# Kernel optimization log

Measured on AMD Instinct MI355X. Metric: run time of the kernel, lower is better.

## Reference

```python
import jax, jax.numpy as jnp
import numpy as np

N_NEG = 60
TEMP = 0.07

def _normalize(x, axis):
    n = jnp.sqrt(jnp.sum(x * x, axis=axis, keepdims=True))
    return x / jnp.maximum(n, 1e-12)

def _grid_sample(img, grid):
    # img [B,C,H,W], grid [B,h,w,2] in [-1,1]; bilinear, padding_mode='border', align_corners=False
    B, C, H, W = img.shape
    ix = jnp.clip((grid[..., 0] + 1.0) * (W * 0.5) - 0.5, 0.0, W - 1.0)
    iy = jnp.clip((grid[..., 1] + 1.0) * (H * 0.5) - 0.5, 0.0, H - 1.0)
    x0 = jnp.floor(ix); y0 = jnp.floor(iy)
    x1 = jnp.minimum(x0 + 1.0, W - 1.0); y1 = jnp.minimum(y0 + 1.0, H - 1.0)
    wx = (ix - x0)[:, None]; wy = (iy - y0)[:, None]  # [B,1,h,w]
    imgf = img.reshape(B, C, H * W)
    hh, ww = grid.shape[1], grid.shape[2]
    def gat(yy, xx):
        idx = (yy * W + xx).astype(jnp.int32).reshape(B, 1, hh * ww)
        return jnp.take_along_axis(imgf, idx, axis=2).reshape(B, C, hh, ww)
    v00 = gat(y0, x0); v01 = gat(y0, x1); v10 = gat(y1, x0); v11 = gat(y1, x1)
    return (v00 * (1 - wx) * (1 - wy) + v01 * wx * (1 - wy)
            + v10 * (1 - wx) * wy + v11 * wx * wy)

def _forward(ref_fms, tgt_fms, target_l, target_r, queue):
    b, c, h, w = ref_fms.shape
    s = target_l.shape[-1] // w  # integer downscale factor (nearest interpolate == strided slice)
    disps_l = target_l[:, :, ::s, ::s] / float(s)   # [b,1,h,w]
    disps_r = target_r[:, :, ::s, ::s] / float(s)
    xb = jnp.broadcast_to(jnp.linspace(0.0, 1.0, w), (b, h, w))
    yb = jnp.broadcast_to(jnp.linspace(0.0, 1.0, h)[:, None], (b, h, w))

    def warp(img, disp):
        g = jnp.stack([xb + disp[:, 0] / w, yb], axis=-1)
        return _grid_sample(img, 2.0 * g - 1.0)

    # occlusion / validity mask (detached in the original)
    index = jnp.broadcast_to(jnp.arange(w, dtype=ref_fms.dtype), (b, 1, h, w))
    l2r2l = warp(warp(index, disps_r), -disps_l)
    masko = jnp.abs(index - l2r2l)[:, 0] < 3.0
    mask = masko & (disps_l[:, 0] > 0.0) & (xb - disps_l[:, 0] / w >= 0.0)
    mask = jax.lax.stop_gradient(mask).astype(ref_fms.dtype)  # [b,h,w]

    query = _normalize(ref_fms, 1)
    # positive: warp right feature to left view via disparity
    gpos = jnp.stack([xb - disps_l[:, 0] / w, yb], axis=-1)
    positive = _normalize(_grid_sample(tgt_fms, 2.0 * gpos - 1.0), 1)
    l_pos = jnp.einsum('bchw,bchw->bhw', query, positive)[..., None]

    # negatives: random integer pixel shifts around positive location
    # (no n_neg-fold repeat of tgt_fms; vmap grid_sample over the n axis instead)
    k1, k2 = jax.random.split(jax.random.key(1234))
    mag = jax.random.randint(k1, (b, h, w, N_NEG), 1, 25).astype(ref_fms.dtype)
    sgn = jnp.sign(jax.random.uniform(k2, (b, h, w, N_NEG)) - 0.5).astype(ref_fms.dtype)
    x_right = (xb - disps_l[:, 0] / w) * w
    fx = jnp.mod(x_right[..., None] + mag * sgn, float(w)) / w
    fy = fx / h  # faithful to original code (y coord reuses the normalized x coord)
    grids = jnp.moveaxis(jnp.stack([fx, fy], axis=-1), 3, 0)  # [n,b,h,w,2]
    neg = jax.vmap(lambda g: _grid_sample(tgt_fms, 2.0 * g - 1.0))(grids)  # [n,b,c,h,w]
    neg = _normalize(jnp.moveaxis(neg, 0, -1), 1)  # [b,c,h,w,n]
    l_neg = jnp.einsum('bchw,bchwn->bhwn', query, neg)

    qn = _normalize(queue, 0)  # forward re-normalizes the queue each call
    l_q = jnp.einsum('bchw,ck->bhwk', query, jax.lax.stop_gradient(qn))

    logits = jnp.concatenate([l_pos, l_neg, l_q], axis=-1) * mask[..., None]
    logits = logits.reshape(b * h * w, -1) / TEMP
    # CrossEntropyLoss with all-zero labels (positive is class 0)
    return jnp.mean(-jax.nn.log_softmax(logits, axis=-1)[:, 0])

def setup_inputs():
    key = jax.random.key(0)
    k1, k2, k3, k4, k5 = jax.random.split(key, 5)
    b, c, h, w = 2, 128, 64, 128
    H, W = 4 * h, 4 * w
    return {
        'ref_fms': jax.random.normal(k1, (b, c, h, w), jnp.float32),
        'tgt_fms': jax.random.normal(k2, (b, c, h, w), jnp.float32),
        'target_l': jax.random.uniform(k3, (b, 1, H, W), jnp.float32) * 64.0,
        'target_r': jax.random.uniform(k4, (b, 1, H, W), jnp.float32) * 64.0,
        'queue': jax.random.normal(k5, (c, 6000), jnp.float32),
    }

def reference(ref_fms, tgt_fms, target_l, target_r, queue):
    return _forward(ref_fms, tgt_fms, target_l, target_r, queue)
```

## Files before the change

### kernel.cpp

```cpp
#include <hip/hip_runtime.h>
#include <stdint.h>
#include <math.h>

#define HFM 64
#define WFM 128
#define CFM 128
#define BN 2
#define HWFM (HFM*WFM)
#define NPIX (BN*HWFM)
#define KQ 6000
#define KQP 6144
#define NNEG 60
#define NE (NPIX*NNEG)
#define EHALF_U 491520u
#define MSHIFT 15.0f
#define LOG2E 1.4426950408889634f

typedef _Float16 f16_8 __attribute__((ext_vector_type(8)));
typedef _Float16 f16_2 __attribute__((ext_vector_type(2)));
typedef float f32_4 __attribute__((ext_vector_type(4)));

__host__ __device__ __forceinline__ void threefry2x32(uint32_t k0, uint32_t k1,
                                                      uint32_t x0, uint32_t x1,
                                                      uint32_t* o0, uint32_t* o1) {
  uint32_t ks2 = k0 ^ k1 ^ 0x1BD11BDAu;
  x0 += k0; x1 += k1;
#define TFR(r) { x0 += x1; x1 = (x1 << (r)) | (x1 >> (32 - (r))); x1 ^= x0; }
  TFR(13) TFR(15) TFR(26) TFR(6)
  x0 += k1;  x1 += ks2 + 1u;
  TFR(17) TFR(29) TFR(16) TFR(24)
  x0 += ks2; x1 += k0 + 2u;
  TFR(13) TFR(15) TFR(26) TFR(6)
  x0 += k0;  x1 += k1 + 3u;
  TFR(17) TFR(29) TFR(16) TFR(24)
  x0 += k1;  x1 += ks2 + 4u;
  TFR(13) TFR(15) TFR(26) TFR(6)
  x0 += ks2; x1 += k0 + 5u;
#undef TFR
  *o0 = x0; *o1 = x1;
}

__device__ __forceinline__ void gs_coord(float t, float halfdim, float maxc,
                                         int* i0, int* i1, float* w) {
  float g = 2.0f * t - 1.0f;
  float x = (g + 1.0f) * halfdim - 0.5f;
  x = fminf(fmaxf(x, 0.0f), maxc);
  float f = floorf(x);
  *i0 = (int)f;
  *w = x - f;
  *i1 = (int)fminf(f + 1.0f, maxc);
}

__global__ __launch_bounds__(256) void k_A(
    const float* __restrict__ ref, const float* __restrict__ tgt,
    const float* __restrict__ queue,
    const float* __restrict__ target_l, const float* __restrict__ target_r,
    _Float16* __restrict__ refTf, _Float16* __restrict__ tgtTf,
    _Float16* __restrict__ queueTf, float2* __restrict__ qeb,
    float* __restrict__ maskArr, float* __restrict__ xr,
    double* __restrict__ dacc, int* __restrict__ dctr) {
  __shared__ float tile[64][35];
  int blk = blockIdx.x;
  int tid = threadIdx.x;
  if (blk < 64) {
    int p = blk * 256 + tid;
    int b = p >> 13;
    int rem = p & (HWFM - 1);
    int i = rem >> 7, j = rem & 127;
    const float stepx = 1.0f / 127.0f, stepy = 1.0f / 63.0f;
    float xb = (j == 127) ? 1.0f : j * stepx;
    float yb = (i == 63) ? 1.0f : i * stepy;
    const float* tl = target_l + (size_t)b * 256 * 512;
    const float* tr = target_r + (size_t)b * 256 * 512;
    float dl = tl[(4 * i) * 512 + 4 * j] * 0.25f;
    int y0i, y1i; float wy;
    gs_coord(yb, 32.0f, 63.0f, &y0i, &y1i, &wy);
    float t = xb - dl * (1.0f / 128.0f);
    int x0i, x1i; float wx;
    gs_coord(t, 64.0f, 127.0f, &x0i, &x1i, &wx);
    auto innerv = [&](int y, int x) -> float {
      float xbx = (x == 127) ? 1.0f : x * stepx;
      float drv = tr[(4 * y) * 512 + 4 * x] * 0.25f;
      float ti = xbx + drv * (1.0f / 128.0f);
      float g = 2.0f * ti - 1.0f;
      float ix2 = fminf(fmaxf((g + 1.0f) * 64.0f - 0.5f, 0.0f), 127.0f);
      float x0f = floorf(ix2);
      float wxp = ix2 - x0f;
      float x1f = fminf(x0f + 1.0f, 127.0f);
      return x0f * (1.0f - wxp) + x1f * wxp;
    };
    float v00 = innerv(y0i, x0i), v01 = innerv(y0i, x1i);
    float v10 = innerv(y1i, x0i), v11 = innerv(y1i, x1i);
    float l2r2l = v00 * (1.0f - wx) * (1.0f - wy) + v01 * wx * (1.0f - wy)
                + v10 * (1.0f - wx) * wy + v11 * wx * wy;
    bool masko = fabsf((float)j - l2r2l) < 3.0f;
    bool mk = masko && (dl > 0.0f) && (t >= 0.0f);
    maskArr[p] = mk ? 1.0f : 0.0f;
    xr[p] = t * 128.0f;
  } else if (blk < 88) {
    if (blk == 64 && tid == 0) { *dacc = 0.0; *dctr = 0; }
    int k = (blk - 64) * 256 + tid;
    if (k < KQP) {
      if (k >= KQ) { qeb[k] = make_float2(0.0f, -1000.0f); }
      else {
        float ss = 0.0f;
        for (int c = 0; c < CFM; c++) { float v = queue[c * KQ + k]; ss += v * v; }
        float qi = 1.0f / fmaxf(sqrtf(ss), 1e-12f);
        qeb[k] = make_float2(qi * (LOG2E / 0.07f), -MSHIFT * LOG2E);
      }
    }
  } else if (blk < 472) {
    int q = blk - 88;
    int cy = q / 192, nx = q - cy * 192;
    int n0 = nx * 32, c0 = cy * 64;
    int c = tid >> 2, qq = tid & 3;
    const float* sp = queue + (size_t)(c0 + c) * KQ + n0 + qq * 4;
    if (n0 + 32 <= KQ) {
      float4 v0 = *(const float4*)sp;
      float4 v1 = *(const float4*)(sp + 16);
      tile[c][qq * 4 + 0] = v0.x; tile[c][qq * 4 + 1] = v0.y;
      tile[c][qq * 4 + 2] = v0.z; tile[c][qq * 4 + 3] = v0.w;
      tile[c][qq * 4 + 16] = v1.x; tile[c][qq * 4 + 17] = v1.y;
      tile[c][qq * 4 + 18] = v1.z; tile[c][qq * 4 + 19] = v1.w;
    } else {
#pragma unroll
      for (int k = 0; k < 4; k++) {
        int n = n0 + qq * 4 + k;
        tile[c][qq * 4 + k] = (n < KQ) ? sp[k] : 0.0f;
        tile[c][qq * 4 + 16 + k] = (n + 16 < KQ) ? sp[16 + k] : 0.0f;
      }
    }
    __syncthreads();
    int x = tid >> 3, j8 = tid & 7;
    f16_8 o;
#pragma unroll
    for (int k = 0; k < 8; k++) o[k] = (_Float16)tile[j8 * 8 + k][x];
    *(f16_8*)(queueTf + (size_t)(n0 + x) * CFM + c0 + j8 * 8) = o;
  } else {
    int fblk = blk - 472;
    int z = fblk >> 9, rem2 = fblk & 511;
    int cy = rem2 >> 8, xt = rem2 & 255;
    int x0 = xt * 32, c0 = cy * 64;
    int arr = z >> 1, b = z & 1;
    const float* src = (arr == 0 ? ref : tgt) + (size_t)b * CFM * HWFM;
    _Float16* dst = (arr == 0 ? refTf : tgtTf) + (size_t)b * HWFM * CFM;
    int c = tid >> 2, qq = tid & 3;
    const float* sp = src + (size_t)(c0 + c) * HWFM + x0 + qq * 4;
    float4 v0 = *(const float4*)sp;
    float4 v1 = *(const float4*)(sp + 16);
    tile[c][qq * 4 + 0] = v0.x; tile[c][qq * 4 + 1] = v0.y;
    tile[c][qq * 4 + 2] = v0.z; tile[c][qq * 4 + 3] = v0.w;
    tile[c][qq * 4 + 16] = v1.x; tile[c][qq * 4 + 17] = v1.y;
    tile[c][qq * 4 + 18] = v1.z; tile[c][qq * 4 + 19] = v1.w;
    __syncthreads();
    int x = tid >> 3, j8 = tid & 7;
    f16_8 o;
#pragma unroll
    for (int k = 0; k < 8; k++) o[k] = (_Float16)tile[j8 * 8 + k][x];
    *(f16_8*)(dst + (size_t)(x0 + x) * CFM + c0 + j8 * 8) = o;
  }
}

__global__ __launch_bounds__(256) void k_B(
    const _Float16* __restrict__ refTf, const _Float16* __restrict__ tgtTf,
    _Float16* __restrict__ QTf, float* __restrict__ stats,
    const float* __restrict__ maskArr, const float* __restrict__ xr,
    float* __restrict__ S, float* __restrict__ logit0,
    int* __restrict__ count, int* __restrict__ list) {
  __shared__ int wsum[4];
  int blk = blockIdx.x;
  int tid = threadIdx.x;
  int lane = tid & 63;
  if (blk == 0) {
    int wave = tid >> 6;
    int base_p = tid * 64;
    unsigned long long bits = 0ull;
    const float4* m4 = (const float4*)(maskArr + base_p);
#pragma unroll
    for (int k = 0; k < 16; k++) {
      float4 v = m4[k];
      if (v.x > 0.0f) bits |= 1ull << (4 * k + 0);
      if (v.y > 0.0f) bits |= 1ull << (4 * k + 1);
      if (v.z > 0.0f) bits |= 1ull << (4 * k + 2);
      if (v.w > 0.0f) bits |= 1ull << (4 * k + 3);
    }
    int m = __popcll(bits);
    int scan = m;
#pragma unroll
    for (int off = 1; off < 64; off <<= 1) {
      int n = __shfl_up(scan, off, 64);
      if (lane >= off) scan += n;
    }
    if (lane == 63) wsum[wave] = scan;
    __syncthreads();
    int wbase = 0;
    for (int w = 0; w < wave; w++) wbase += wsum[w];
    int idx = wbase + scan - m;
    for (int k = 0; k < 64; k++) {
      if ((bits >> k) & 1ull) list[idx++] = base_p + k;
    }
    if (tid == 255) *count = idx;
  } else if (blk < 65) {
    int sub = tid >> 6;
    int xg = (blk - 1) * 4 + sub;
    int b = xg >> 7, x = xg & 127;
    int xp = min(x + 1, 127);
    int c2 = lane * 2;
    int base = b * HWFM;
    f16_2 c0  = *(const f16_2*)(tgtTf + (size_t)(base + x) * CFM + c2);
    f16_2 c1  = *(const f16_2*)(tgtTf + (size_t)(base + WFM + x) * CFM + c2);
    f16_2 c0p = *(const f16_2*)(tgtTf + (size_t)(base + xp) * CFM + c2);
    f16_2 c1p = *(const f16_2*)(tgtTf + (size_t)(base + WFM + xp) * CFM + c2);
    float a0 = (float)c0[0], a1 = (float)c0[1];
    float b0 = (float)c1[0], b1 = (float)c1[1];
    float p0 = (float)c0p[0], p1 = (float)c0p[1];
    float q0 = (float)c1p[0], q1 = (float)c1p[1];
    float s[7];
    s[0] = a0 * a0 + a1 * a1;
    s[1] = a0 * b0 + a1 * b1;
    s[2] = b0 * b0 + b1 * b1;
    s[3] = a0 * p0 + a1 * p1;
    s[4] = a0 * q0 + a1 * q1;
    s[5] = b0 * p0 + b1 * p1;
    s[6] = b0 * q0 + b1 * q1;
#pragma unroll
    for (int o = 32; o; o >>= 1)
#pragma unroll
      for (int k = 0; k < 7; k++) s[k] += __shfl_xor(s[k], o, 64);
    if (lane == 0) {
      float* st = stats + (size_t)xg * 8;
#pragma unroll
      for (int k = 0; k < 7; k++) st[k] = s[k];
      st[7] = 0.0f;
    }
  } else {
    int wave = tid >> 6;
    int p = (blk - 65) * 4 + wave;
    float mk = maskArr[p];
    if (mk == 0.0f) return;
    int b = p >> 13;
    int rem = p & (HWFM - 1);
    int i = rem >> 7;
    const float stepy = 1.0f / 63.0f;
    float yb = (i == 63) ? 1.0f : i * stepy;
    float t = xr[p] * (1.0f / 128.0f);
    int y0i, y1i; float wy;
    gs_coord(yb, 32.0f, 63.0f, &y0i, &y1i, &wy);
    int x0i, x1i; float wx;
    gs_coord(t, 64.0f, 127.0f, &x0i, &x1i, &wx);

    int c2 = lane * 2;
    f16_2 q2 = *(const f16_2*)(refTf + (size_t)p * CFM + c2);
    int bo = b * HWFM;
    f16_2 a2 = *(const f16_2*)(tgtTf + (size_t)(bo + y0i * WFM + x0i) * CFM + c2);
    f16_2 b2 = *(const f16_2*)(tgtTf + (size_t)(bo + y0i * WFM + x1i) * CFM + c2);
    f16_2 cc2 = *(const f16_2*)(tgtTf + (size_t)(bo + y1i * WFM + x0i) * CFM + c2);
    f16_2 d2 = *(const f16_2*)(tgtTf + (size_t)(bo + y1i * WFM + x1i) * CFM + c2);

    float w00 = (1.0f - wx) * (1.0f - wy), w01 = wx * (1.0f - wy);
    float w10 = (1.0f - wx) * wy,          w11 = wx * wy;
    float q0 = (float)q2[0], q1 = (float)q2[1];
    float v0 = w00 * (float)a2[0] + w01 * (float)b2[0] + w10 * (float)cc2[0] + w11 * (float)d2[0];
    float v1 = w00 * (float)a2[1] + w01 * (float)b2[1] + w10 * (float)cc2[1] + w11 * (float)d2[1];

    float s0 = q0 * q0 + q1 * q1;
    float s1 = q0 * v0 + q1 * v1;
    float s2 = v0 * v0 + v1 * v1;
#pragma unroll
    for (int o = 32; o; o >>= 1) {
      s0 += __shfl_xor(s0, o, 64);
      s1 += __shfl_xor(s1, o, 64);
      s2 += __shfl_xor(s2, o, 64);
    }
    float inv = 1.0f / fmaxf(sqrtf(s0), 1e-12f);
    f16_2 qw; qw[0] = (_Float16)(q0 * inv); qw[1] = (_Float16)(q1 * inv);
    *(f16_2*)(QTf + (size_t)p * CFM + c2) = qw;
    if (lane == 0) {
      float lpos = (s1 * inv) / fmaxf(sqrtf(s2), 1e-12f);
      float lg0 = lpos / 0.07f;
      logit0[p] = lg0;
      S[p] = expf(lg0 - MSHIFT);
    }
  }
}

__global__ __launch_bounds__(256, 4) void k_gemm(
    const _Float16* __restrict__ QTf,
    const _Float16* __restrict__ queueTf,
    const _Float16* __restrict__ tgtTf,
    const float2* __restrict__ qeb,
    float* __restrict__ S, float* __restrict__ D,
    const int* __restrict__ count, const int* __restrict__ list) {
  __shared__ _Float16 Bs[2][64 * CFM];
  __shared__ float Srow[64];
  int tid = threadIdx.x;
  int cnt = *count;
  int split = blockIdx.x & 7;
  int slot0 = (blockIdx.x >> 3) * 64;
  if (slot0 >= cnt) return;
  int wave = tid >> 6, lane = tid & 63;
  int quad = lane >> 4, l16 = lane & 15;
  int wm = wave >> 1, wn = wave & 1;
  int dbatch = split >> 2;
  int dxoff = (split & 3) * 64;

  if (tid < 64) Srow[tid] = 0.0f;

  int lrow = lane >> 4, lchunk = lane & 15;
  auto stage = [&](const _Float16* bsrc, int buf) {
#pragma unroll
    for (int i = 0; i < 4; i++) {
      int rb = wave * 16 + i * 4;
      int r = rb + lrow;
      const _Float16* g = bsrc + (size_t)r * CFM + ((lchunk ^ (r & 7)) << 3);
      __builtin_amdgcn_global_load_lds(
          (const __attribute__((address_space(1))) void*)g,
          (__attribute__((address_space(3))) void*)(&Bs[buf][rb * CFM]),
          16, 0, 0);
    }
  };
  auto bpanel = [&](int ic) -> const _Float16* {
    if (ic < 12) return queueTf + (size_t)(split * 768 + ic * 64) * CFM;
    return tgtTf + ((size_t)dbatch * HWFM + dxoff) * CFM;
  };

  stage(bpanel(0), 0);

  f16_8 Af[2][4];
  int r0 = slot0 + wm * 32;
#pragma unroll
  for (int mt = 0; mt < 2; mt++) {
    int prow = list[min(r0 + mt * 16 + l16, cnt - 1)];
    const _Float16* arow = QTf + (size_t)prow * CFM + quad * 8;
#pragma unroll
    for (int ks = 0; ks < 4; ks++)
      Af[mt][ks] = *(const f16_8*)(arow + ks * 32);
  }
  int pbv[2][4];
#pragma unroll
  for (int mt = 0; mt < 2; mt++)
#pragma unroll
    for (int r = 0; r < 4; r++)
      pbv[mt][r] = list[min(r0 + mt * 16 + quad * 4 + r, cnt - 1)] >> 13;

  __syncthreads();
  int cur = 0;
  float rowsum[2][4] = {{0.0f,0.0f,0.0f,0.0f},{0.0f,0.0f,0.0f,0.0f}};

  for (int ic = 0; ic < 13; ic++) {
    if (ic + 1 < 13) stage(bpanel(ic + 1), cur ^ 1);
    float2 qb[2];
    if (ic < 12) {
      int n0 = split * 768 + ic * 64 + wn * 32;
#pragma unroll
      for (int nt = 0; nt < 2; nt++) qb[nt] = qeb[n0 + nt * 16 + l16];
    }
    f32_4 acc[2][2];
#pragma unroll
    for (int mt = 0; mt < 2; mt++)
#pragma unroll
      for (int nt = 0; nt < 2; nt++)
        acc[mt][nt] = (f32_4){0.0f, 0.0f, 0.0f, 0.0f};
#pragma unroll
    for (int ks = 0; ks < 4; ks++) {
      f16_8 Bk[2];
#pragma unroll
      for (int nt = 0; nt < 2; nt++) {
        int brow = wn * 32 + nt * 16 + l16;
        Bk[nt] = *(const f16_8*)(&Bs[cur][brow * CFM + ((ks * 32 + quad * 8) ^ ((brow & 7) * 8))]);
      }
#pragma unroll
      for (int mt = 0; mt < 2; mt++)
#pragma unroll
        for (int nt = 0; nt < 2; nt++)
          acc[mt][nt] = __builtin_amdgcn_mfma_f32_16x16x32_f16(Af[mt][ks], Bk[nt], acc[mt][nt], 0, 0, 0);
    }
    if (ic < 12) {
#pragma unroll
      for (int nt = 0; nt < 2; nt++)
#pragma unroll
        for (int mt = 0; mt < 2; mt++)
#pragma unroll
          for (int r = 0; r < 4; r++)
            rowsum[mt][r] += exp2f(fmaf(acc[mt][nt][r], qb[nt].x, qb[nt].y));
    } else {
#pragma unroll
      for (int mt = 0; mt < 2; mt++)
#pragma unroll
        for (int nt = 0; nt < 2; nt++)
#pragma unroll
          for (int r = 0; r < 4; r++) {
            int sl = slot0 + wm * 32 + mt * 16 + quad * 4 + r;
            int colL = dxoff + wn * 32 + nt * 16 + l16;
            if (sl < cnt && pbv[mt][r] == dbatch)
              D[(size_t)sl * 256 + colL] = acc[mt][nt][r];
          }
    }
    __syncthreads();
    cur ^= 1;
  }

#pragma unroll
  for (int mt = 0; mt < 2; mt++)
#pragma unroll
    for (int r = 0; r < 4; r++) {
      float vv = rowsum[mt][r];
      vv += __shfl_xor(vv, 1);
      vv += __shfl_xor(vv, 2);
      vv += __shfl_xor(vv, 4);
      vv += __shfl_xor(vv, 8);
      rowsum[mt][r] = vv;
    }
  if (l16 == 0) {
#pragma unroll
    for (int mt = 0; mt < 2; mt++)
#pragma unroll
      for (int r = 0; r < 4; r++)
        atomicAdd(&Srow[wm * 32 + mt * 16 + quad * 4 + r], rowsum[mt][r]);
  }
  __syncthreads();
  if (tid < 64) {
    int pr = slot0 + tid;
    if (pr < cnt) atomicAdd(&S[list[pr]], Srow[tid]);
  }
}

__global__ __launch_bounds__(256) void k_negatives_lite(
    const float* __restrict__ D, const float* __restrict__ stats,
    const float* __restrict__ xr, float* __restrict__ S,
    const int* __restrict__ count, const int* __restrict__ list,
    uint32_t k1a, uint32_t k1b, uint32_t k2a, uint32_t k2b) {
  int tid = threadIdx.x;
  int wave = tid >> 6, lane = tid & 63;
  int cnt = *count;
  int slot = blockIdx.x * 4 + wave;
  if (slot >= cnt) return;
  int p = list[slot];
  int b = p >> 13;
  float esum = 0.0f;
  if (lane < NNEG) {
    uint32_t e = (uint32_t)(p * NNEG + lane);
    uint32_t h0, h1;
    threefry2x32(k1a, k1b, e, e + (uint32_t)NE, &h0, &h1);
    uint32_t off = ((h0 % 24u) * 16u + (h1 % 24u)) % 24u;
    float mag = (float)(1u + off);
    uint32_t ub;
    {
      uint32_t a, bm;
      if (e < EHALF_U) { threefry2x32(k2a, k2b, e, e + EHALF_U, &a, &bm); ub = a; }
      else             { threefry2x32(k2a, k2b, e - EHALF_U, e, &a, &bm); ub = bm; }
    }
    float u = __uint_as_float((ub >> 9) | 0x3F800000u) - 1.0f;
    float sg = (u > 0.5f) ? 1.0f : ((u < 0.5f) ? -1.0f : 0.0f);

    float v = xr[p] + mag * sg;
    float r = fmodf(v, 128.0f);
    if (r < 0.0f) r += 128.0f;
    float fx = r * (1.0f / 128.0f);
    float fy = fx * (1.0f / 64.0f);
    int x0i, x1i, y0i, y1i; float wx, wy;
    gs_coord(fx, 64.0f, 127.0f, &x0i, &x1i, &wx);
    gs_coord(fy, 32.0f, 63.0f, &y0i, &y1i, &wy);

    const float* Dp = D + (size_t)slot * 256;
    float d00 = Dp[x0i], d01 = Dp[x1i];
    float d10 = Dp[128 + x0i], d11 = Dp[128 + x1i];
    float u0 = 1.0f - wy, u1 = wy;
    float dv0 = u0 * d00 + u1 * d10;
    float dv1 = u0 * d01 + u1 * d11;
    float dot = (1.0f - wx) * dv0 + wx * dv1;

    const float* st0 = stats + (size_t)(b * 128 + x0i) * 8;
    const float* st1 = stats + (size_t)(b * 128 + x1i) * 8;
    float4 sa = *(const float4*)st0;
    float4 sb = *(const float4*)(st0 + 4);
    float4 sc = *(const float4*)st1;
    float a0 = u0 * u0, a1 = u0 * u1, a2 = u1 * u1;
    float nB0 = a0 * sa.x + 2.0f * a1 * sa.y + a2 * sa.z;
    float nB1 = a0 * sc.x + 2.0f * a1 * sc.y + a2 * sc.z;
    float cB  = a0 * sa.w + a1 * (sb.x + sb.y) + a2 * sb.z;
    float wx0 = 1.0f - wx;
    float nsq = wx0 * wx0 * nB0 + 2.0f * wx * wx0 * cB + wx * wx * nB1;
    float ln = dot / fmaxf(sqrtf(fmaxf(nsq, 0.0f)), 1e-12f);
    esum = __expf(ln * (1.0f / 0.07f) - MSHIFT);
  }
#pragma unroll
  for (int o = 32; o; o >>= 1) esum += __shfl_xor(esum, o, 64);
  if (lane == 0) atomicAdd(&S[p], esum);
}

__global__ __launch_bounds__(1024) void k_finalize(
    const float* __restrict__ S, const float* __restrict__ logit0,
    const float* __restrict__ maskArr, float* __restrict__ out,
    double* __restrict__ dacc, int* __restrict__ dctr) {
  int tid = threadIdx.x;
  const float cmask = logf(6061.0f);
  int p = blockIdx.x * 1024 + tid;
  float term = (maskArr[p] > 0.0f) ? (logf(S[p]) + MSHIFT - logit0[p]) : cmask;
  double acc = (double)term;
#pragma unroll
  for (int off = 32; off; off >>= 1) acc += __shfl_down(acc, off, 64);
  __shared__ double sd[16];
  if ((tid & 63) == 0) sd[tid >> 6] = acc;
  __syncthreads();
  if (tid == 0) {
    double tot = 0.0;
    for (int w = 0; w < 16; w++) tot += sd[w];
    atomicAdd(dacc, tot);
    __threadfence();
    int old = atomicAdd(dctr, 1);
    if (old == 15) {
      __threadfence();
      out[0] = (float)(*(volatile double*)dacc / (double)NPIX);
    }
  }
}

extern "C" void kernel_launch(void* const* d_in, const int* in_sizes, int n_in,
                              void* d_out, int out_size, void* d_ws, size_t ws_size,
                              hipStream_t stream) {
  const float* ref   = (const float*)d_in[0];
  const float* tgt   = (const float*)d_in[1];
  const float* tl    = (const float*)d_in[2];
  const float* tr    = (const float*)d_in[3];
  const float* queue = (const float*)d_in[4];
  float* out = (float*)d_out;
  float* ws = (float*)d_ws;

  float2* qeb = (float2*)ws;
  float* S    = ws + 12288;
  float* lg0  = ws + 28672;
  float* mk   = ws + 45056;
  float* xr   = ws + 61440;
  int* count  = (int*)(ws + 77824);
  double* dacc = (double*)(ws + 77826);
  int* dctr   = (int*)(ws + 77828);
  int* list   = (int*)(ws + 77840);
  _Float16* QTf     = (_Float16*)(ws + 94464);
  _Float16* queueTf = (_Float16*)(ws + 1143040);
  _Float16* tgtTf   = (_Float16*)(ws + 1536256);
  _Float16* refTf   = (_Float16*)(ws + 2584832);
  float* stats = ws + 3633408;
  float* D     = ws + 3635456;

  uint32_t b0o0, b0o1, b1o0, b1o1;
  threefry2x32(0u, 1234u, 0u, 2u, &b0o0, &b0o1);
  threefry2x32(0u, 1234u, 1u, 3u, &b1o0, &b1o1);
  uint32_t k1a = b0o0, k1b = b1o0, k2a = b0o1, k2b = b1o1;

  k_A<<<dim3(2520), dim3(256), 0, stream>>>(ref, tgt, queue, tl, tr,
                                            refTf, tgtTf, queueTf, qeb, mk, xr,
                                            dacc, dctr);
  k_B<<<dim3(65 + 4096), dim3(256), 0, stream>>>(refTf, tgtTf, QTf, stats,
                                                 mk, xr, S, lg0, count, list);
  k_gemm<<<dim3(2048), dim3(256), 0, stream>>>(QTf, queueTf, tgtTf, qeb,
                                               S, D, count, list);
  k_negatives_lite<<<dim3(NPIX / 4), dim3(256), 0, stream>>>(D, stats, xr, S, count, list,
                                                             k1a, k1b, k2a, k2b);
  k_finalize<<<dim3(16), dim3(1024), 0, stream>>>(S, lg0, mk, out, dacc, dctr);
}
```

Baseline: 115.9 us.

## Parallelize mask compaction with atomics and split GEMM queue columns across more blocks

Replaces the single-block serial compaction of masked pixels with 64 blocks that each use a wave ballot, a popcount prefix and one atomicAdd per wave to append to the active list. The counter is zeroed in k_A. The GEMM grid is doubled to 16 splits per 64-row slot, each covering 384 queue columns instead of 768. Only the first 8 splits also compute the D tile against the target features. The aim is to remove the one-block serial bottleneck in k_B and raise GEMM parallelism, at the cost of a nondeterministic list order and more A-panel reloads.

```diff
diff --git a/kernel.cpp b/kernel.cpp
--- a/kernel.cpp
+++ b/kernel.cpp
@@ -58,7 +58,7 @@
     _Float16* __restrict__ refTf, _Float16* __restrict__ tgtTf,
     _Float16* __restrict__ queueTf, float2* __restrict__ qeb,
     float* __restrict__ maskArr, float* __restrict__ xr,
-    double* __restrict__ dacc, int* __restrict__ dctr) {
+    double* __restrict__ dacc, int* __restrict__ dctr, int* __restrict__ count) {
   __shared__ float tile[64][35];
   int blk = blockIdx.x;
   int tid = threadIdx.x;
@@ -98,7 +98,7 @@
     maskArr[p] = mk ? 1.0f : 0.0f;
     xr[p] = t * 128.0f;
   } else if (blk < 88) {
-    if (blk == 64 && tid == 0) { *dacc = 0.0; *dctr = 0; }
+    if (blk == 64 && tid == 0) { *dacc = 0.0; *dctr = 0; *count = 0; }
     int k = (blk - 64) * 256 + tid;
     if (k < KQP) {
       if (k >= KQ) { qeb[k] = make_float2(0.0f, -1000.0f); }
@@ -167,42 +167,22 @@
     const float* __restrict__ maskArr, const float* __restrict__ xr,
     float* __restrict__ S, float* __restrict__ logit0,
     int* __restrict__ count, int* __restrict__ list) {
-  __shared__ int wsum[4];
   int blk = blockIdx.x;
   int tid = threadIdx.x;
   int lane = tid & 63;
-  if (blk == 0) {
-    int wave = tid >> 6;
-    int base_p = tid * 64;
-    unsigned long long bits = 0ull;
-    const float4* m4 = (const float4*)(maskArr + base_p);
-#pragma unroll
-    for (int k = 0; k < 16; k++) {
-      float4 v = m4[k];
-      if (v.x > 0.0f) bits |= 1ull << (4 * k + 0);
-      if (v.y > 0.0f) bits |= 1ull << (4 * k + 1);
-      if (v.z > 0.0f) bits |= 1ull << (4 * k + 2);
-      if (v.w > 0.0f) bits |= 1ull << (4 * k + 3);
-    }
-    int m = __popcll(bits);
-    int scan = m;
-#pragma unroll
-    for (int off = 1; off < 64; off <<= 1) {
-      int n = __shfl_up(scan, off, 64);
-      if (lane >= off) scan += n;
-    }
-    if (lane == 63) wsum[wave] = scan;
-    __syncthreads();
-    int wbase = 0;
-    for (int w = 0; w < wave; w++) wbase += wsum[w];
-    int idx = wbase + scan - m;
-    for (int k = 0; k < 64; k++) {
-      if ((bits >> k) & 1ull) list[idx++] = base_p + k;
-    }
-    if (tid == 255) *count = idx;
-  } else if (blk < 65) {
+  if (blk < 64) {
+    int p = blk * 256 + tid;
+    bool m = maskArr[p] > 0.0f;
+    unsigned long long bits = __ballot(m);
+    int nact = __popcll(bits);
+    int prefix = __popcll(bits & ((1ull << lane) - 1ull));
+    int base = 0;
+    if (lane == 0 && nact) base = atomicAdd(count, nact);
+    base = __shfl(base, 0, 64);
+    if (m) list[base + prefix] = p;
+  } else if (blk < 128) {
     int sub = tid >> 6;
-    int xg = (blk - 1) * 4 + sub;
+    int xg = (blk - 64) * 4 + sub;
     int b = xg >> 7, x = xg & 127;
     int xp = min(x + 1, 127);
     int c2 = lane * 2;
@@ -235,7 +215,7 @@
     }
   } else {
     int wave = tid >> 6;
-    int p = (blk - 65) * 4 + wave;
+    int p = (blk - 128) * 4 + wave;
     float mk = maskArr[p];
     if (mk == 0.0f) return;
     int b = p >> 13;
@@ -295,12 +275,14 @@
   __shared__ float Srow[64];
   int tid = threadIdx.x;
   int cnt = *count;
-  int split = blockIdx.x & 7;
-  int slot0 = (blockIdx.x >> 3) * 64;
+  int split = blockIdx.x & 15;
+  int slot0 = (blockIdx.x >> 4) * 64;
   if (slot0 >= cnt) return;
   int wave = tid >> 6, lane = tid & 63;
   int quad = lane >> 4, l16 = lane & 15;
   int wm = wave >> 1, wn = wave & 1;
+  bool hasD = (split < 8);
+  int nc = hasD ? 7 : 6;
   int dbatch = split >> 2;
   int dxoff = (split & 3) * 64;
 
@@ -320,7 +302,7 @@
     }
   };
   auto bpanel = [&](int ic) -> const _Float16* {
-    if (ic < 12) return queueTf + (size_t)(split * 768 + ic * 64) * CFM;
+    if (ic < 6) return queueTf + (size_t)(split * 384 + ic * 64) * CFM;
     return tgtTf + ((size_t)dbatch * HWFM + dxoff) * CFM;
   };
 
@@ -337,21 +319,23 @@
       Af[mt][ks] = *(const f16_8*)(arow + ks * 32);
   }
   int pbv[2][4];
-#pragma unroll
-  for (int mt = 0; mt < 2; mt++)
-#pragma unroll
-    for (int r = 0; r < 4; r++)
-      pbv[mt][r] = list[min(r0 + mt * 16 + quad * 4 + r, cnt - 1)] >> 13;
+  if (hasD) {
+#pragma unroll
+    for (int mt = 0; mt < 2; mt++)
+#pragma unroll
+      for (int r = 0; r < 4; r++)
+        pbv[mt][r] = list[min(r0 + mt * 16 + quad * 4 + r, cnt - 1)] >> 13;
+  }
 
   __syncthreads();
   int cur = 0;
   float rowsum[2][4] = {{0.0f,0.0f,0.0f,0.0f},{0.0f,0.0f,0.0f,0.0f}};
 
-  for (int ic = 0; ic < 13; ic++) {
-    if (ic + 1 < 13) stage(bpanel(ic + 1), cur ^ 1);
+  for (int ic = 0; ic < nc; ic++) {
+    if (ic + 1 < nc) stage(bpanel(ic + 1), cur ^ 1);
     float2 qb[2];
-    if (ic < 12) {
-      int n0 = split * 768 + ic * 64 + wn * 32;
+    if (ic < 6) {
+      int n0 = split * 384 + ic * 64 + wn * 32;
 #pragma unroll
       for (int nt = 0; nt < 2; nt++) qb[nt] = qeb[n0 + nt * 16 + l16];
     }
@@ -375,7 +359,7 @@
         for (int nt = 0; nt < 2; nt++)
           acc[mt][nt] = __builtin_amdgcn_mfma_f32_16x16x32_f16(Af[mt][ks], Bk[nt], acc[mt][nt], 0, 0, 0);
     }
-    if (ic < 12) {
+    if (ic < 6) {
 #pragma unroll
       for (int nt = 0; nt < 2; nt++)
 #pragma unroll
@@ -550,10 +534,10 @@
 
   k_A<<<dim3(2520), dim3(256), 0, stream>>>(ref, tgt, queue, tl, tr,
                                             refTf, tgtTf, queueTf, qeb, mk, xr,
-                                            dacc, dctr);
-  k_B<<<dim3(65 + 4096), dim3(256), 0, stream>>>(refTf, tgtTf, QTf, stats,
-                                                 mk, xr, S, lg0, count, list);
-  k_gemm<<<dim3(2048), dim3(256), 0, stream>>>(QTf, queueTf, tgtTf, qeb,
+                                            dacc, dctr, count);
+  k_B<<<dim3(128 + 4096), dim3(256), 0, stream>>>(refTf, tgtTf, QTf, stats,
+                                                  mk, xr, S, lg0, count, list);
+  k_gemm<<<dim3(4096), dim3(256), 0, stream>>>(QTf, queueTf, tgtTf, qeb,
                                                S, D, count, list);
   k_negatives_lite<<<dim3(NPIX / 4), dim3(256), 0, stream>>>(D, stats, xr, S, count, list,
                                                              k1a, k1b, k2a, k2b);
```

Result: slower. 119.8 us (+3.3%).
